# Kernel optimization log

Measured on AMD Instinct MI355X. Metric: run time of the kernel, lower is better.

Reference implementation:

```python
import jax, jax.numpy as jnp
import numpy as np

N = 50000
E = 600000
D = 128  # hidden_dim


def setup_inputs() -> dict:
    key = jax.random.key(0)
    k_x, k_ei, k_ea, k_w1, k_b1, k_w2, k_b2 = jax.random.split(key, 7)
    x = jax.random.normal(k_x, (N, D), dtype=jnp.float32)
    edge_index = jax.random.randint(k_ei, (2, E), 0, N, dtype=jnp.int64)
    edge_attr = jax.random.normal(k_ea, (E, D), dtype=jnp.float32)
    # torch nn.Linear init scale ~ 1/sqrt(fan_in); stored as [in, out] here
    s1 = 1.0 / np.sqrt(2 * D)
    s2 = 1.0 / np.sqrt(D)
    W1 = jax.random.uniform(k_w1, (2 * D, D), dtype=jnp.float32, minval=-s1, maxval=s1)
    b1 = jax.random.uniform(k_b1, (D,), dtype=jnp.float32, minval=-s1, maxval=s1)
    W2 = jax.random.uniform(k_w2, (D, D), dtype=jnp.float32, minval=-s2, maxval=s2)
    b2 = jax.random.uniform(k_b2, (D,), dtype=jnp.float32, minval=-s2, maxval=s2)
    return {"x": x, "edge_index": edge_index, "edge_attr": edge_attr,
            "W1": W1, "b1": b1, "W2": W2, "b2": b2}


def reference(x, edge_index, edge_attr, W1, b1, W2, b2):
    row, col = edge_index[0], edge_index[1]
    # scatter-add edge features to both endpoints (index_add_ twice)
    edge_aggr = jnp.zeros((x.shape[0], edge_attr.shape[1]), dtype=x.dtype)
    edge_aggr = edge_aggr.at[row].add(edge_attr).at[col].add(edge_attr)
    node_features = jnp.concatenate([x, edge_aggr], axis=1)  # [N, 2D]
    h = jax.nn.relu(node_features @ W1 + b1)
    return h @ W2 + b2
```

## Files before the change

kernel.cpp:

```cpp
#include <hip/hip_runtime.h>

#define D 128

__global__ __launch_bounds__(256) void degree_kernel(
    const int* __restrict__ ei, int* __restrict__ deg, int twoE) {
  int i = blockIdx.x * blockDim.x + threadIdx.x;
  int base = i * 4;
  if (base + 3 < twoE) {
    int4 v = *reinterpret_cast<const int4*>(ei + base);
    atomicAdd(&deg[v.x], 1); atomicAdd(&deg[v.y], 1);
    atomicAdd(&deg[v.z], 1); atomicAdd(&deg[v.w], 1);
  } else {
    for (int j = base; j < twoE; ++j) atomicAdd(&deg[ei[j]], 1);
  }
}

__global__ __launch_bounds__(256) void scan_blocksum(
    const int* __restrict__ deg, int* __restrict__ partials, int n) {
  __shared__ int red[256];
  int t = threadIdx.x;
  int base = blockIdx.x * 1024 + t * 4;
  int s = 0;
#pragma unroll
  for (int j = 0; j < 4; ++j) {
    int i = base + j;
    s += (i < n) ? deg[i] : 0;
  }
  red[t] = s;
  __syncthreads();
#pragma unroll
  for (int w = 128; w > 0; w >>= 1) {
    if (t < w) red[t] += red[t + w];
    __syncthreads();
  }
  if (t == 0) partials[blockIdx.x] = red[0];
}

__global__ __launch_bounds__(64) void scan_partials(int* partials, int nb) {
  __shared__ int tmp[64];
  int t = threadIdx.x;
  int v = (t < nb) ? partials[t] : 0;
  tmp[t] = v;
  __syncthreads();
#pragma unroll
  for (int s = 1; s < 64; s <<= 1) {
    int a = (t >= s) ? tmp[t - s] : 0;
    __syncthreads();
    tmp[t] += a;
    __syncthreads();
  }
  if (t < nb) partials[t] = tmp[t] - v;
}

__global__ __launch_bounds__(256) void scan_final(
    const int* __restrict__ deg, const int* __restrict__ partials,
    int* __restrict__ off, int* __restrict__ cursor, int n) {
  __shared__ int red[256];
  int t = threadIdx.x;
  int base = blockIdx.x * 1024 + t * 4;
  int v[4];
#pragma unroll
  for (int j = 0; j < 4; ++j) v[j] = (base + j < n) ? deg[base + j] : 0;
  int tsum = v[0] + v[1] + v[2] + v[3];
  red[t] = tsum;
  __syncthreads();
#pragma unroll
  for (int s = 1; s < 256; s <<= 1) {
    int a = (t >= s) ? red[t - s] : 0;
    __syncthreads();
    red[t] += a;
    __syncthreads();
  }
  int e = red[t] - tsum + partials[blockIdx.x];
#pragma unroll
  for (int j = 0; j < 4; ++j) {
    if (base + j < n) { off[base + j] = e; cursor[base + j] = e; }
    e += v[j];
  }
}

__global__ __launch_bounds__(256) void fill_kernel(
    const int* __restrict__ ei, int* __restrict__ cursor,
    int* __restrict__ elist, int E, int twoE) {
  int i = blockIdx.x * blockDim.x + threadIdx.x;
  if (i >= twoE) return;
  int node = ei[i];
  int e = (i < E) ? i : i - E;
  int pos = atomicAdd(&cursor[node], 1);
  elist[pos] = e;
}

__global__ __launch_bounds__(128) void gather_kernel(
    const float* __restrict__ edge_attr, const int* __restrict__ off,
    const int* __restrict__ deg, const int* __restrict__ elist,
    float* __restrict__ aggr, int N) {
  int node = blockIdx.x;
  int j = threadIdx.x;
  int s = off[node];
  int d = deg[node];
  float acc = 0.f;
  int k = 0;
  for (; k + 4 <= d; k += 4) {
    int e0 = elist[s + k + 0];
    int e1 = elist[s + k + 1];
    int e2 = elist[s + k + 2];
    int e3 = elist[s + k + 3];
    float v0 = edge_attr[(long long)e0 * D + j];
    float v1 = edge_attr[(long long)e1 * D + j];
    float v2 = edge_attr[(long long)e2 * D + j];
    float v3 = edge_attr[(long long)e3 * D + j];
    acc += (v0 + v1) + (v2 + v3);
  }
  for (; k < d; ++k) {
    int e = elist[s + k];
    acc += edge_attr[(long long)e * D + j];
  }
  aggr[(long long)node * D + j] = acc;
}

__global__ __launch_bounds__(256) void fused_mlp(
    const float* __restrict__ x, const float* __restrict__ aggr,
    const float* __restrict__ W1, const float* __restrict__ b1,
    const float* __restrict__ W2, const float* __restrict__ b2,
    float* __restrict__ outp, int N) {
  constexpr int KC = 64;
  __shared__ float Ws[KC][D];
  __shared__ float AsHs[64 * D];
  const int t = threadIdx.x;
  const int tx = t & 31;
  const int ty = t >> 5;
  const int row0 = blockIdx.x * 64;
  const int col = tx * 4;

  float acc[8][4];
  {
    float4 b = reinterpret_cast<const float4*>(b1)[tx];
#pragma unroll
    for (int i = 0; i < 8; ++i) {
      acc[i][0] = b.x; acc[i][1] = b.y; acc[i][2] = b.z; acc[i][3] = b.w;
    }
  }

  for (int kc = 0; kc < 256; kc += KC) {
#pragma unroll
    for (int p = 0; p < 4; ++p) {
      int r = p * 16 + (t >> 4);
      int c4 = (t & 15);
      int gk = kc + c4 * 4;
      int gr = row0 + r;
      float4 v = make_float4(0.f, 0.f, 0.f, 0.f);
      if (gr < N) {
        const float* src = (gk < 128) ? (x + (long long)gr * 128 + gk)
                                      : (aggr + (long long)gr * 128 + (gk - 128));
        v = *reinterpret_cast<const float4*>(src);
      }
      *reinterpret_cast<float4*>(&AsHs[r * KC + c4 * 4]) = v;
    }
#pragma unroll
    for (int p = 0; p < 8; ++p) {
      int r = p * 8 + (t >> 5);
      float4 v = *reinterpret_cast<const float4*>(W1 + (long long)(kc + r) * D + (t & 31) * 4);
      *reinterpret_cast<float4*>(&Ws[r][(t & 31) * 4]) = v;
    }
    __syncthreads();
#pragma unroll
    for (int k4 = 0; k4 < KC / 4; ++k4) {
      float4 wv[4];
#pragma unroll
      for (int kk = 0; kk < 4; ++kk)
        wv[kk] = *reinterpret_cast<const float4*>(&Ws[k4 * 4 + kk][col]);
#pragma unroll
      for (int i = 0; i < 8; ++i) {
        float4 av = *reinterpret_cast<const float4*>(&AsHs[(ty * 8 + i) * KC + k4 * 4]);
        acc[i][0] += av.x * wv[0].x + av.y * wv[1].x + av.z * wv[2].x + av.w * wv[3].x;
        acc[i][1] += av.x * wv[0].y + av.y * wv[1].y + av.z * wv[2].y + av.w * wv[3].y;
        acc[i][2] += av.x * wv[0].z + av.y * wv[1].z + av.z * wv[2].z + av.w * wv[3].z;
        acc[i][3] += av.x * wv[0].w + av.y * wv[1].w + av.z * wv[2].w + av.w * wv[3].w;
      }
    }
    __syncthreads();
  }

#pragma unroll
  for (int i = 0; i < 8; ++i) {
    float4 o = make_float4(fmaxf(acc[i][0], 0.f), fmaxf(acc[i][1], 0.f),
                           fmaxf(acc[i][2], 0.f), fmaxf(acc[i][3], 0.f));
    *reinterpret_cast<float4*>(&AsHs[(ty * 8 + i) * D + col]) = o;
  }

  {
    float4 b = reinterpret_cast<const float4*>(b2)[tx];
#pragma unroll
    for (int i = 0; i < 8; ++i) {
      acc[i][0] = b.x; acc[i][1] = b.y; acc[i][2] = b.z; acc[i][3] = b.w;
    }
  }
  for (int kc = 0; kc < 128; kc += KC) {
#pragma unroll
    for (int p = 0; p < 8; ++p) {
      int r = p * 8 + (t >> 5);
      float4 v = *reinterpret_cast<const float4*>(W2 + (long long)(kc + r) * D + (t & 31) * 4);
      *reinterpret_cast<float4*>(&Ws[r][(t & 31) * 4]) = v;
    }
    __syncthreads();
#pragma unroll
    for (int k4 = 0; k4 < KC / 4; ++k4) {
      float4 wv[4];
#pragma unroll
      for (int kk = 0; kk < 4; ++kk)
        wv[kk] = *reinterpret_cast<const float4*>(&Ws[k4 * 4 + kk][col]);
#pragma unroll
      for (int i = 0; i < 8; ++i) {
        float4 av = *reinterpret_cast<const float4*>(&AsHs[(ty * 8 + i) * D + kc + k4 * 4]);
        acc[i][0] += av.x * wv[0].x + av.y * wv[1].x + av.z * wv[2].x + av.w * wv[3].x;
        acc[i][1] += av.x * wv[0].y + av.y * wv[1].y + av.z * wv[2].y + av.w * wv[3].y;
        acc[i][2] += av.x * wv[0].z + av.y * wv[1].z + av.z * wv[2].z + av.w * wv[3].z;
        acc[i][3] += av.x * wv[0].w + av.y * wv[1].w + av.z * wv[2].w + av.w * wv[3].w;
      }
    }
    __syncthreads();
  }

#pragma unroll
  for (int i = 0; i < 8; ++i) {
    int gr = row0 + ty * 8 + i;
    if (gr < N) {
      float4 o = make_float4(acc[i][0], acc[i][1], acc[i][2], acc[i][3]);
      reinterpret_cast<float4*>(outp + (long long)gr * D)[tx] = o;
    }
  }
}

extern "C" void kernel_launch(void* const* d_in, const int* in_sizes, int n_in,
                              void* d_out, int out_size, void* d_ws, size_t ws_size,
                              hipStream_t stream) {
  const float* x         = (const float*)d_in[0];
  const int*   ei        = (const int*)d_in[1];
  const float* edge_attr = (const float*)d_in[2];
  const float* W1        = (const float*)d_in[3];
  const float* b1        = (const float*)d_in[4];
  const float* W2        = (const float*)d_in[5];
  const float* b2        = (const float*)d_in[6];
  const int N = in_sizes[0] / D;
  const int E = in_sizes[2] / D;
  const int twoE = 2 * E;

  float* aggr   = (float*)d_ws;
  int* deg      = (int*)(aggr + (size_t)N * D);
  int* off      = deg + N;
  int* cursor   = off + N;
  int* partials = cursor + N;
  int* elist    = partials + 64;

  const int nb = (N + 1023) / 1024;

  hipMemsetAsync(deg, 0, (size_t)N * sizeof(int), stream);

  degree_kernel<<<(twoE / 4 + 255) / 256, 256, 0, stream>>>(ei, deg, twoE);
  scan_blocksum<<<nb, 256, 0, stream>>>(deg, partials, N);
  scan_partials<<<1, 64, 0, stream>>>(partials, nb);
  scan_final<<<nb, 256, 0, stream>>>(deg, partials, off, cursor, N);
  fill_kernel<<<(twoE + 255) / 256, 256, 0, stream>>>(ei, cursor, elist, E, twoE);
  gather_kernel<<<N, 128, 0, stream>>>(edge_attr, off, deg, elist, aggr, N);

  int gb = (N + 63) / 64;
  fused_mlp<<<gb, 256, 0, stream>>>(x, aggr, W1, b1, W2, b2, (float*)d_out, N);
}
```

Before: 819.1 us.

## Read MLP weights from global memory directly and batch gather over two nodes

The fused MLP no longer stages W1/W2 tiles in shared memory. Each thread loads its weight float4s straight from global (cached) memory, which frees LDS and removes barriers so more blocks can be resident (launch_bounds min 4 blocks). The gather kernel now processes two nodes per 256-thread block and unrolls the edge loop to 8 loads for more memory-level parallelism. The trade-off is that weight reads now hit L1/L2 per thread instead of being shared through LDS, which may raise global load traffic and latency in the inner loop.

```diff
diff --git a/kernel.cpp b/kernel.cpp
--- a/kernel.cpp
+++ b/kernel.cpp
@@ -90,26 +90,26 @@
   elist[pos] = e;
 }
 
-__global__ __launch_bounds__(128) void gather_kernel(
+__global__ __launch_bounds__(256) void gather_kernel(
     const float* __restrict__ edge_attr, const int* __restrict__ off,
     const int* __restrict__ deg, const int* __restrict__ elist,
     float* __restrict__ aggr, int N) {
-  int node = blockIdx.x;
-  int j = threadIdx.x;
+  int node = blockIdx.x * 2 + (threadIdx.x >> 7);
+  int j = threadIdx.x & 127;
+  if (node >= N) return;
   int s = off[node];
   int d = deg[node];
   float acc = 0.f;
   int k = 0;
-  for (; k + 4 <= d; k += 4) {
-    int e0 = elist[s + k + 0];
-    int e1 = elist[s + k + 1];
-    int e2 = elist[s + k + 2];
-    int e3 = elist[s + k + 3];
-    float v0 = edge_attr[(long long)e0 * D + j];
-    float v1 = edge_attr[(long long)e1 * D + j];
-    float v2 = edge_attr[(long long)e2 * D + j];
-    float v3 = edge_attr[(long long)e3 * D + j];
-    acc += (v0 + v1) + (v2 + v3);
+  for (; k + 8 <= d; k += 8) {
+    int e[8];
+#pragma unroll
+    for (int u = 0; u < 8; ++u) e[u] = elist[s + k + u];
+    float v[8];
+#pragma unroll
+    for (int u = 0; u < 8; ++u) v[u] = edge_attr[(long long)e[u] * D + j];
+#pragma unroll
+    for (int u = 0; u < 8; ++u) acc += v[u];
   }
   for (; k < d; ++k) {
     int e = elist[s + k];
@@ -118,13 +118,12 @@
   aggr[(long long)node * D + j] = acc;
 }
 
-__global__ __launch_bounds__(256) void fused_mlp(
+__global__ __launch_bounds__(256, 4) void fused_mlp(
     const float* __restrict__ x, const float* __restrict__ aggr,
     const float* __restrict__ W1, const float* __restrict__ b1,
     const float* __restrict__ W2, const float* __restrict__ b2,
     float* __restrict__ outp, int N) {
   constexpr int KC = 64;
-  __shared__ float Ws[KC][D];
   __shared__ float AsHs[64 * D];
   const int t = threadIdx.x;
   const int tx = t & 31;
@@ -134,7 +133,7 @@
 
   float acc[8][4];
   {
-    float4 b = reinterpret_cast<const float4*>(b1)[tx];
+    float4 b = *reinterpret_cast<const float4*>(b1 + col);
 #pragma unroll
     for (int i = 0; i < 8; ++i) {
       acc[i][0] = b.x; acc[i][1] = b.y; acc[i][2] = b.z; acc[i][3] = b.w;
@@ -156,26 +155,23 @@
       }
       *reinterpret_cast<float4*>(&AsHs[r * KC + c4 * 4]) = v;
     }
-#pragma unroll
-    for (int p = 0; p < 8; ++p) {
-      int r = p * 8 + (t >> 5);
-      float4 v = *reinterpret_cast<const float4*>(W1 + (long long)(kc + r) * D + (t & 31) * 4);
-      *reinterpret_cast<float4*>(&Ws[r][(t & 31) * 4]) = v;
-    }
-    __syncthreads();
+    __syncthreads();
+
+    const float* Wp = W1 + (long long)kc * D + col;
 #pragma unroll
     for (int k4 = 0; k4 < KC / 4; ++k4) {
-      float4 wv[4];
-#pragma unroll
-      for (int kk = 0; kk < 4; ++kk)
-        wv[kk] = *reinterpret_cast<const float4*>(&Ws[k4 * 4 + kk][col]);
+      float4 wv0 = *reinterpret_cast<const float4*>(Wp + 0 * D);
+      float4 wv1 = *reinterpret_cast<const float4*>(Wp + 1 * D);
+      float4 wv2 = *reinterpret_cast<const float4*>(Wp + 2 * D);
+      float4 wv3 = *reinterpret_cast<const float4*>(Wp + 3 * D);
+      Wp += 4 * D;
 #pragma unroll
       for (int i = 0; i < 8; ++i) {
         float4 av = *reinterpret_cast<const float4*>(&AsHs[(ty * 8 + i) * KC + k4 * 4]);
-        acc[i][0] += av.x * wv[0].x + av.y * wv[1].x + av.z * wv[2].x + av.w * wv[3].x;
-        acc[i][1] += av.x * wv[0].y + av.y * wv[1].y + av.z * wv[2].y + av.w * wv[3].y;
-        acc[i][2] += av.x * wv[0].z + av.y * wv[1].z + av.z * wv[2].z + av.w * wv[3].z;
-        acc[i][3] += av.x * wv[0].w + av.y * wv[1].w + av.z * wv[2].w + av.w * wv[3].w;
+        acc[i][0] += av.x * wv0.x + av.y * wv1.x + av.z * wv2.x + av.w * wv3.x;
+        acc[i][1] += av.x * wv0.y + av.y * wv1.y + av.z * wv2.y + av.w * wv3.y;
+        acc[i][2] += av.x * wv0.z + av.y * wv1.z + av.z * wv2.z + av.w * wv3.z;
+        acc[i][3] += av.x * wv0.w + av.y * wv1.w + av.z * wv2.w + av.w * wv3.w;
       }
     }
     __syncthreads();
@@ -187,38 +183,33 @@
                            fmaxf(acc[i][2], 0.f), fmaxf(acc[i][3], 0.f));
     *reinterpret_cast<float4*>(&AsHs[(ty * 8 + i) * D + col]) = o;
   }
+  __syncthreads();
 
   {
-    float4 b = reinterpret_cast<const float4*>(b2)[tx];
+    float4 b = *reinterpret_cast<const float4*>(b2 + col);
 #pragma unroll
     for (int i = 0; i < 8; ++i) {
       acc[i][0] = b.x; acc[i][1] = b.y; acc[i][2] = b.z; acc[i][3] = b.w;
     }
   }
-  for (int kc = 0; kc < 128; kc += KC) {
-#pragma unroll
-    for (int p = 0; p < 8; ++p) {
-      int r = p * 8 + (t >> 5);
-      float4 v = *reinterpret_cast<const float4*>(W2 + (long long)(kc + r) * D + (t & 31) * 4);
-      *reinterpret_cast<float4*>(&Ws[r][(t & 31) * 4]) = v;
-    }
-    __syncthreads();
-#pragma unroll
-    for (int k4 = 0; k4 < KC / 4; ++k4) {
-      float4 wv[4];
-#pragma unroll
-      for (int kk = 0; kk < 4; ++kk)
-        wv[kk] = *reinterpret_cast<const float4*>(&Ws[k4 * 4 + kk][col]);
+  {
+    const float* Wp = W2 + col;
+#pragma unroll
+    for (int k4 = 0; k4 < 32; ++k4) {
+      float4 wv0 = *reinterpret_cast<const float4*>(Wp + 0 * D);
+      float4 wv1 = *reinterpret_cast<const float4*>(Wp + 1 * D);
+      float4 wv2 = *reinterpret_cast<const float4*>(Wp + 2 * D);
+      float4 wv3 = *reinterpret_cast<const float4*>(Wp + 3 * D);
+      Wp += 4 * D;
 #pragma unroll
       for (int i = 0; i < 8; ++i) {
-        float4 av = *reinterpret_cast<const float4*>(&AsHs[(ty * 8 + i) * D + kc + k4 * 4]);
-        acc[i][0] += av.x * wv[0].x + av.y * wv[1].x + av.z * wv[2].x + av.w * wv[3].x;
-        acc[i][1] += av.x * wv[0].y + av.y * wv[1].y + av.z * wv[2].y + av.w * wv[3].y;
-        acc[i][2] += av.x * wv[0].z + av.y * wv[1].z + av.z * wv[2].z + av.w * wv[3].z;
-        acc[i][3] += av.x * wv[0].w + av.y * wv[1].w + av.z * wv[2].w + av.w * wv[3].w;
+        float4 av = *reinterpret_cast<const float4*>(&AsHs[(ty * 8 + i) * D + k4 * 4]);
+        acc[i][0] += av.x * wv0.x + av.y * wv1.x + av.z * wv2.x + av.w * wv3.x;
+        acc[i][1] += av.x * wv0.y + av.y * wv1.y + av.z * wv2.y + av.w * wv3.y;
+        acc[i][2] += av.x * wv0.z + av.y * wv1.z + av.z * wv2.z + av.w * wv3.z;
+        acc[i][3] += av.x * wv0.w + av.y * wv1.w + av.z * wv2.w + av.w * wv3.w;
       }
     }
-    __syncthreads();
   }
 
 #pragma unroll
@@ -261,8 +252,7 @@
   scan_partials<<<1, 64, 0, stream>>>(partials, nb);
   scan_final<<<nb, 256, 0, stream>>>(deg, partials, off, cursor, N);
   fill_kernel<<<(twoE + 255) / 256, 256, 0, stream>>>(ei, cursor, elist, E, twoE);
-  gather_kernel<<<N, 128, 0, stream>>>(edge_attr, off, deg, elist, aggr, N);
-
-  int gb = (N + 63) / 64;
-  fused_mlp<<<gb, 256, 0, stream>>>(x, aggr, W1, b1, W2, b2, (float*)d_out, N);
-}
+  gather_kernel<<<(N + 1) / 2, 256, 0, stream>>>(edge_attr, off, deg, elist, aggr, N);
+
+  fused_mlp<<<(N + 63) / 64, 256, 0, stream>>>(x, aggr, W1, b1, W2, b2, (float*)d_out, N);
+}
```

Measured after the change: 2.760 ms. 237% more time.
